# Kernel optimization log

Hardware: AMD Instinct MI355X
Metric: run time of the kernel (lower is better)

## Reference

```python
import jax, jax.numpy as jnp
import numpy as np

N_QUBITS = 12
BATCH = 2048
N_CLASSES = 10


def build_tape(n):
    # 2 layers of: RX on all wires (id 0), RY (id 1), RZ (id 2), then a CRX ring
    # (id 4 forward in layer 0, id 5 reversed in layer 1). 96 gates total for n=12.
    tape = []
    for layer in range(2):
        for i in range(n):
            tape.append(("rx", (i,)))
        for i in range(n):
            tape.append(("ry", (i,)))
        for i in range(n):
            tape.append(("rz", (i,)))
        order = range(n) if layer == 0 else range(n - 1, -1, -1)
        for i in order:
            tape.append(("crx", (i, (i + 1) % n)))
    return tape


def rx_mat(t):
    c = jnp.cos(t / 2).astype(jnp.complex64)
    s = jnp.sin(t / 2).astype(jnp.complex64)
    return jnp.stack([jnp.stack([c, -1j * s]), jnp.stack([-1j * s, c])])


def ry_mat(t):
    c = jnp.cos(t / 2).astype(jnp.complex64)
    s = jnp.sin(t / 2).astype(jnp.complex64)
    return jnp.stack([jnp.stack([c, -s]), jnp.stack([s, c])])


def rz_mat(t):
    em = jnp.exp(-1j * t.astype(jnp.complex64) / 2)
    ep = jnp.exp(1j * t.astype(jnp.complex64) / 2)
    z = jnp.zeros((), jnp.complex64)
    return jnp.stack([jnp.stack([em, z]), jnp.stack([z, ep])])


def apply_1q(psi, U, w):
    # psi: [B] + [2]*n, gate on wire w (axis 1+w)
    psi = jnp.moveaxis(psi, 1 + w, -1)
    psi = psi @ U.T
    return jnp.moveaxis(psi, -1, 1 + w)


def apply_crx(psi, theta, c, t):
    a_c, a_t = 1 + c, 1 + t
    psi = jnp.moveaxis(psi, a_c, 1)  # control -> axis 1
    if a_t < a_c:
        a_t += 1
    psi = jnp.moveaxis(psi, a_t, -1)  # target -> last axis
    U = rx_mat(theta)
    p1 = psi[:, 1] @ U.T  # apply RX only on control=1 branch
    psi = jnp.stack([psi[:, 0], p1], axis=1)
    psi = jnp.moveaxis(psi, -1, a_t)
    return jnp.moveaxis(psi, 1, a_c)


def expvals(psi, n):
    # <X_i>, <Y_i>, <Z_i> for each qubit; returns [B, 3n] ordered X..Y..Z (PL order)
    xs, ys, zs = [], [], []
    for i in range(n):
        p = jnp.moveaxis(psi, 1 + i, -1).reshape(psi.shape[0], -1, 2)
        z = jnp.sum(jnp.abs(p[..., 0]) ** 2 - jnp.abs(p[..., 1]) ** 2, axis=1)
        cross = jnp.sum(jnp.conj(p[..., 0]) * p[..., 1], axis=1)
        xs.append(2.0 * jnp.real(cross))
        ys.append(2.0 * jnp.imag(cross))
        zs.append(jnp.real(z))
    return jnp.stack(xs + ys + zs, axis=1).astype(jnp.float32)


def setup_inputs() -> dict:
    key = jax.random.key(0)
    k0, k1, k2 = jax.random.split(key, 3)
    sv = jax.random.normal(k0, (BATCH, 2 ** N_QUBITS), dtype=jnp.float32)
    sv = sv / jnp.linalg.norm(sv, axis=1, keepdims=True)  # valid quantum states
    n_gates = len(build_tape(N_QUBITS))
    angles = jax.random.normal(k1, (n_gates,), dtype=jnp.float32)
    W = jax.random.normal(k2, (N_CLASSES, 3 * N_QUBITS), dtype=jnp.float32) * 0.1
    b = jnp.zeros((N_CLASSES,), jnp.float32)
    return {"state_vectors": sv, "angles": angles, "W": W, "b": b}


def reference(state_vectors, angles, W, b):
    tape = build_tape(N_QUBITS)
    psi = state_vectors.astype(jnp.complex64).reshape((-1,) + (2,) * N_QUBITS)
    for g, (kind, wires) in enumerate(tape):
        th = angles[g]
        if kind == "rx":
            psi = apply_1q(psi, rx_mat(th), wires[0])
        elif kind == "ry":
            psi = apply_1q(psi, ry_mat(th), wires[0])
        elif kind == "rz":
            psi = apply_1q(psi, rz_mat(th), wires[0])
        else:
            psi = apply_crx(psi, th, wires[0], wires[1])
    feats = expvals(psi, N_QUBITS)  # [B, 3*n_qubits]
    return feats @ W.T + b
```

## Files before the change

### kernel.cpp

```cpp
#include <hip/hip_runtime.h>

#define DIM 4096
using F2 = float2;
using F8 = __attribute__((ext_vector_type(8))) float;
using F2V = __attribute__((ext_vector_type(2))) float;


__device__ __forceinline__ F8 sld8(const float* p) {
    F8 r;
    asm volatile("s_load_dwordx8 %0, %1, 0x0\n\ts_waitcnt lgkmcnt(0)"
                 : "=s"(r) : "s"(p));
    return r;
}
__device__ __forceinline__ void sld16(const float* pa, const float* pb, F8& a, F8& b) {
    asm volatile("s_load_dwordx8 %0, %2, 0x0\n\t"
                 "s_load_dwordx8 %1, %3, 0x0\n\t"
                 "s_waitcnt lgkmcnt(0)"
                 : "=&s"(a), "=&s"(b) : "s"(pa), "s"(pb));
}
__device__ __forceinline__ F2 sld2(const float* p) {
    F2V r;
    asm volatile("s_load_dwordx2 %0, %1, 0x0\n\ts_waitcnt lgkmcnt(0)"
                 : "=s"(r) : "s"(p));
    return F2{r[0], r[1]};
}

__device__ __forceinline__ F2 pk_mul_bl(F2 a, F2 u) {
    F2 d;
    asm("v_pk_mul_f32 %0, %1, %2 op_sel:[0,0] op_sel_hi:[1,0]"
        : "=v"(d) : "v"(a), "s"(u));
    return d;
}
__device__ __forceinline__ void pk_cross(F2& d, F2 a, F2 u) {
    asm("v_pk_fma_f32 %0, %1, %2, %0 op_sel:[1,1,0] op_sel_hi:[0,1,1] neg_lo:[1,0,0]"
        : "+v"(d) : "v"(a), "s"(u));
}
__device__ __forceinline__ void pk_fma_bl(F2& d, F2 a, F2 u) {
    asm("v_pk_fma_f32 %0, %1, %2, %0 op_sel:[0,0,0] op_sel_hi:[1,0,1]"
        : "+v"(d) : "v"(a), "s"(u));
}
__device__ __forceinline__ void pk_swapneg(F2& d, F2 a, F2 cs) {
    asm("v_pk_fma_f32 %0, %1, %2, %0 op_sel:[1,1,0] op_sel_hi:[0,1,1] neg_hi:[1,0,0]"
        : "+v"(d) : "v"(a), "s"(cs));
}
__device__ __forceinline__ void pk_fma(F2& d, F2 a, F2 b) {
    asm("v_pk_fma_f32 %0, %1, %2, %0" : "+v"(d) : "v"(a), "v"(b));
}
__device__ __forceinline__ void pk_imacc(F2& d, F2 a0, F2 a1) {
    asm("v_pk_fma_f32 %0, %1, %2, %0 op_sel:[0,1,0] op_sel_hi:[1,0,1] neg_hi:[1,0,0]"
        : "+v"(d) : "v"(a0), "v"(a1));
}
__device__ __forceinline__ F2 pk_cmul(F2 u, F2 a) {
    F2 d = pk_mul_bl(a, u);
    pk_cross(d, a, u);
    return d;
}
__device__ __forceinline__ void pk_cfma(F2& d, F2 u, F2 a) {
    pk_fma_bl(d, a, u);
    pk_cross(d, a, u);
}

__device__ __forceinline__ void build_u(float tx, float ty, float tz, float* u) {
    float sx = sinf(0.5f*tx), cx = cosf(0.5f*tx);
    float sy = sinf(0.5f*ty), cy = cosf(0.5f*ty);
    float sz = sinf(0.5f*tz), cz = cosf(0.5f*tz);
    float A00r = cy*cx, A00i =  sy*sx;
    float A01r = -sy*cx, A01i = -cy*sx;
    float A10r =  sy*cx, A10i = -cy*sx;
    float A11r =  cy*cx, A11i = -sy*sx;
    u[0] = cz*A00r + sz*A00i;  u[1] = cz*A00i - sz*A00r;
    u[2] = cz*A01r + sz*A01i;  u[3] = cz*A01i - sz*A01r;
    u[4] = cz*A10r - sz*A10i;  u[5] = cz*A10i + sz*A10r;
    u[6] = cz*A11r - sz*A11i;  u[7] = cz*A11i + sz*A11r;
}

__global__ void prep_kernel(const float* __restrict__ ang, float* __restrict__ coef) {
    int t = threadIdx.x;
    if (t < 12) {
        float u[8]; build_u(ang[t], ang[12+t], ang[24+t], u);
#pragma unroll
        for (int j = 0; j < 8; ++j) coef[t*8 + j] = u[j];
    } else if (t < 24) {
        int q = t - 12;
        float u[8]; build_u(ang[48+q], ang[60+q], ang[72+q], u);
#pragma unroll
        for (int j = 0; j < 8; ++j) coef[192 + q*8 + j] = u[j];
    } else if (t < 36) {
        int c = t - 24;
        float th = 0.5f * ang[95 - c];
        coef[296 + c*2]     = cosf(th);
        coef[296 + c*2 + 1] = sinf(th);
    } else if (t < 47) {
        int q = t - 35;
        float u[8]; build_u(ang[q], ang[12+q], ang[24+q], u);
        float c = cosf(0.5f*ang[36+q-1]), s = sinf(0.5f*ang[36+q-1]);
        float m[8];
        m[0] = c*u[0] + s*u[5];  m[1] = c*u[1] - s*u[4];
        m[2] = c*u[2] + s*u[7];  m[3] = c*u[3] - s*u[6];
        m[4] = s*u[1] + c*u[4];  m[5] = -s*u[0] + c*u[5];
        m[6] = s*u[3] + c*u[6];  m[7] = -s*u[2] + c*u[7];
#pragma unroll
        for (int j = 0; j < 8; ++j) coef[96 + q*8 + j] = m[j];
    } else if (t == 47) {
        float u[8]; build_u(ang[48], ang[60], ang[72], u);
        float c = cosf(0.5f*ang[47]), s = sinf(0.5f*ang[47]);
        float m[8];
        m[0] = c*u[0] + s*u[3];  m[1] = c*u[1] - s*u[2];
        m[2] = s*u[1] + c*u[2];  m[3] = -s*u[0] + c*u[3];
        m[4] = c*u[4] + s*u[7];  m[5] = c*u[5] - s*u[6];
        m[6] = s*u[5] + c*u[6];  m[7] = -s*u[4] + c*u[7];
#pragma unroll
        for (int j = 0; j < 8; ++j) coef[288 + j] = m[j];
    }
}

__device__ __forceinline__ int rpA1(int r) {
    int a11=(r>>3)&1, a10=(r>>2)&1, a9=(r>>1)&1;
    return (a11<<8)|(a10<<7)|(a9<<6)|(a11<<3)|(a10<<2)|(a9<<1)|(a9<<0);
}
__device__ __forceinline__ int rpB1(int r) {
    int a5=(r>>1)&1, a7=(r>>2)&1, a6=(r>>3)&1;
    return (a7<<5)|(a6<<4)|(a7<<3)|(a6<<2)|(a5<<0);
}
__device__ __forceinline__ int rpB2(int r) {
    int a8=r&1, a7=(r>>2)&1, a6=(r>>3)&1;
    return (a8<<5)|(a7<<4)|(a6<<3)|(a7<<2)|(a8<<1)|(a6<<0);
}
__device__ __forceinline__ int rpC2(int r) {
    int a2=r&1, a4=(r>>2)&1, a3=(r>>3)&1;
    return (a3<<3)|(a2<<2)|(a4<<1);
}
__device__ __forceinline__ int rpC3(int r) {
    int a5=(r>>1)&1, a4=(r>>2)&1, a3=(r>>3)&1;
    return (a5<<4)|(a3<<3)|(a4<<2)|(a5<<0);
}
__device__ __forceinline__ int rpD3(int r) {
    int a1=(r>>1)&1, a0=(r>>2)&1, a11=(r>>3)&1;
    return (a11<<8)|(a11<<3)|(a1<<1)|((a0^a11)<<0);
}
__device__ __forceinline__ int rpC5(int r) {
    int a2=r&1, a4=(r>>2)&1, a3=(r>>3)&1;
    return (a4<<4)|(a3<<3)|(a2<<2)|(a4<<0);
}
__device__ __forceinline__ int rpB5(int r) {
    int a8=r&1, a7=(r>>2)&1, a6=(r>>3)&1;
    return (a7<<10)|(a6<<9)|(a8<<5)|(a8<<3);
}

#define LBITS \
    const int l0=l&1, l1=(l>>1)&1, l2=(l>>2)&1, l3=(l>>3)&1, l4=(l>>4)&1, \
              l5=(l>>5)&1, w0=w&1, w1=(w>>1)&1; \
    (void)l0;(void)l1;(void)l2;(void)l3;(void)l4;(void)l5;(void)w0;(void)w1;

__device__ __forceinline__ int tpA1f(int l, int w) { LBITS
    return (w1<<10)|(w0<<9)|(l5<<5)|(l4<<4)|((l1^l5)<<3)|((l0^l4)<<2)|(l2<<1)|(l3<<0); }
__device__ __forceinline__ int tpB1f(int l, int w) { LBITS
    return (w1<<10)|(w0<<9)|(l5<<8)|(l4<<7)|(l3<<6)|((l1^l5)<<3)|((l0^l4)<<2)|((l2^l3)<<1)|(l3<<0); }
__device__ __forceinline__ int tpC2f(int l, int w) { LBITS
    return (w1<<10)|(w0<<9)|(l5<<8)|(l4<<7)|(l3<<6)|(l2<<5)|(l1<<4)|((l5^l0)<<3)|((l4^l1)<<2)|((l3^l2)<<1)|((l0^l3)<<0); }
__device__ __forceinline__ int tpC3f(int l, int w) { LBITS
    return (l1<<10)|(l0<<9)|(l5<<8)|(l4<<7)|(l3<<6)|(l2<<5)|((l5^l4)<<3)|(l3<<2)|((w1^l2)<<1)|((w0^l5)<<0); }
__device__ __forceinline__ int tpD3f(int l, int w) { LBITS
    return (w1<<10)|(w0<<9)|(l5<<7)|(l4<<6)|(l3<<5)|(l2<<4)|((l0^l5)<<3)|((l1^l4)<<2)|(l3<<1)|(l2<<0); }
__device__ __forceinline__ int tpC4f(int l, int w) { LBITS
    return (w1<<10)|(w0<<9)|(l5<<8)|(l4<<7)|(l3<<6)|(l2<<5)|((l5^l4)<<3)|(l3<<2)|((l1^l2)<<1)|((l0^l5)<<0); }
__device__ __forceinline__ int tpC5f(int l, int w) { LBITS
    return (w1<<10)|(w0<<9)|(l5<<8)|(l4<<7)|(l3<<6)|(l2<<5)|((l5^l2)<<3)|(l4<<2)|((l1^l3)<<1)|(l0<<0); }
__device__ __forceinline__ int tpB5f(int l, int w) { LBITS
    return (l5<<8)|(l4<<7)|(l3<<6)|(l2<<4)|((l1^l5)<<3)|((l0^l4)<<2)|((w1^l3)<<1)|((w0^l2)<<0); }

template<int M, int S1, int H1>
__device__ __forceinline__ void g1q(F2* amp, F2 u00, F2 u01, F2 u10, F2 u11) {
#pragma unroll
    for (int r0 = 0; r0 < 16; ++r0) {
        if (r0 & M) continue;
        if (S1 != 0 && (r0 & S1) != H1) continue;
        const int r1 = r0 + M;
        F2 a0 = amp[r0], a1 = amp[r1];
        F2 n0 = pk_cmul(u00, a0); pk_cfma(n0, u01, a1);
        F2 n1 = pk_cmul(u10, a0); pk_cfma(n1, u11, a1);
        amp[r0] = n0; amp[r1] = n1;
    }
}
template<int M, int S1, int H1>
__device__ __forceinline__ void g1qF(F2* amp, F8 u) {
    g1q<M, S1, H1>(amp, F2{u[0],u[1]}, F2{u[2],u[3]}, F2{u[4],u[5]}, F2{u[6],u[7]});
}

template<int MSEL, int M, int S1, int H1>
__device__ __forceinline__ void fg1q(F2* amp, F2 a00, F2 a01, F2 a10, F2 a11,
                                     F2 b00, F2 b01, F2 b10, F2 b11) {
#pragma unroll
    for (int r0 = 0; r0 < 16; ++r0) {
        if (r0 & M) continue;
        if (S1 != 0 && (r0 & S1) != H1) continue;
        const int r1 = r0 + M;
        const bool sel = (r0 & MSEL) != 0;
        F2 u00 = sel ? b00 : a00, u01 = sel ? b01 : a01;
        F2 u10 = sel ? b10 : a10, u11 = sel ? b11 : a11;
        F2 a0 = amp[r0], a1 = amp[r1];
        F2 n0 = pk_cmul(u00, a0); pk_cfma(n0, u01, a1);
        F2 n1 = pk_cmul(u10, a0); pk_cfma(n1, u11, a1);
        amp[r0] = n0; amp[r1] = n1;
    }
}
template<int MSEL, int M, int S1, int H1>
__device__ __forceinline__ void fg1qF(F2* amp, F8 a, F8 b) {
    fg1q<MSEL, M, S1, H1>(amp,
        F2{a[0],a[1]}, F2{a[2],a[3]}, F2{a[4],a[5]}, F2{a[6],a[7]},
        F2{b[0],b[1]}, F2{b[2],b[3]}, F2{b[4],b[5]}, F2{b[6],b[7]});
}

template<int MC, int MT>
__device__ __forceinline__ void crx(F2* amp, F2 cs) {
#pragma unroll
    for (int r0 = 0; r0 < 16; ++r0) {
        if (!(r0 & MC) || (r0 & MT)) continue;
        const int r1 = r0 + MT;
        F2 a0 = amp[r0], a1 = amp[r1];
        F2 n0 = pk_mul_bl(a0, cs); pk_swapneg(n0, a1, cs);
        F2 n1 = pk_mul_bl(a1, cs); pk_swapneg(n1, a0, cs);
        amp[r0] = n0; amp[r1] = n1;
    }
}

template<int M>
__device__ __forceinline__ void expv(const F2* amp, int q, int lane,
                                     float& fx, float& fy, float& fz) {
    F2 zp = {0.f, 0.f}, zm = {0.f, 0.f}, xp = {0.f, 0.f}, ip = {0.f, 0.f};
#pragma unroll
    for (int r0 = 0; r0 < 16; ++r0) {
        if (r0 & M) continue;
        const int r1 = r0 + M;
        F2 a0 = amp[r0], a1 = amp[r1];
        pk_fma(zp, a0, a0);
        pk_fma(zm, a1, a1);
        pk_fma(xp, a0, a1);
        pk_imacc(ip, a0, a1);
    }
    float zz = (zp.x + zp.y) - (zm.x + zm.y);
    float xr = 2.f * (xp.x + xp.y);
    float xi = 2.f * (ip.x + ip.y);
#pragma unroll
    for (int off = 32; off; off >>= 1) {
        xr += __shfl_xor(xr, off);
        xi += __shfl_xor(xi, off);
        zz += __shfl_xor(zz, off);
    }
    if (lane == q) { fx = xr; fy = xi; fz = zz; }
}

template<int M, int SB>
__device__ __forceinline__ int r0_of(int j, int hb) {
    int r = hb ? SB : 0, b = 1;
#pragma unroll
    for (int p = 0; p < 4; ++p) {
        const int mm = 1 << p;
        if (mm == M || mm == SB) continue;
        if (j & b) r |= mm;
        b <<= 1;
    }
    return r;
}

#define ST_T(TP, RP, SB, HB) \
  { _Pragma("unroll") for (int r = 0; r < 16; ++r) { \
      if ((r & (SB)) != (HB)) continue; \
      psi[(TP) ^ RP(r)] = amp[r]; } }
#define LD_T(TP, RP, M, SB, HB) \
  { _Pragma("unroll") for (int k = 0; k < 8; ++k) { \
      const int j = k >> 1; \
      const int r0 = r0_of<M, SB>(j, (HB) != 0); \
      const int r = (k & 1) ? (r0 + (M)) : r0; \
      amp[r] = psi[(TP) ^ RP(r)]; } }

#define U0P(q, M)    g1qF<M, 0, 0>(amp, sld8(cf + (q)*8))
#define FU0(q, MS, M) do { F8 ua_, ub_; sld16(cf + (q)*8, cf + 96 + (q)*8, ua_, ub_); \
                           fg1qF<MS, M, 0, 0>(amp, ua_, ub_); } while(0)
#define U1P(q, M)    g1qF<M, 0, 0>(amp, sld8(cf + 192 + (q)*8))
#define FU1_0()      do { F8 ua_, ub_; sld16(cf + 192, cf + 288, ua_, ub_); \
                          fg1qF<4, 8, 0, 0>(amp, ua_, ub_); } while(0)
#define CR1(c, MC, MT) crx<MC, MT>(amp, sld2(cf + 296 + (c)*2))
#define EXPV(q, M)   expv<M>(amp, q, l, fx, fy, fz)

__global__ __launch_bounds__(256, 1)
void qsim_kernel(const float* __restrict__ sv,
                 const float* __restrict__ cf,
                 const float* __restrict__ W,
                 const float* __restrict__ bvec,
                 float* __restrict__ out)
{
    __shared__ F2 psi[2048];
    const int t = threadIdx.x;
    const int b = blockIdx.x;
    const int l = t & 63, w = t >> 6;

    F2 amp[16];
    const float* svb = sv + (size_t)b * DIM;
#pragma unroll
    for (int k = 0; k < 16; ++k) {
        const int r = (k & 1) ? ((k >> 1) + 8) : (k >> 1);
        amp[r] = make_float2(svb[(r << 8) | (l << 2) | w], 0.f);
    }

    float fx = 0.f, fy = 0.f, fz = 0.f;

    U0P(0, 8);
    FU0(1, 8, 4); FU0(2, 4, 2); FU0(3, 2, 1);

    {
        F8 ua, ub; sld16(cf + 4*8, cf + 96 + 4*8, ua, ub);
        const int tpA = tpA1f(l, w), tpB = tpB1f(l, w);
        ST_T(tpA, rpA1, 1, 0);
        LD_T(tpB, rpB1, 4, 1, 0);
        ST_T(tpA, rpA1, 1, 1);
        fg1qF<1, 4, 1, 0>(amp, ua, ub);
        LD_T(tpB, rpB1, 4, 1, 1);
        fg1qF<1, 4, 1, 1>(amp, ua, ub);
    }
    FU0(5, 4, 8); FU0(6, 8, 2);

    {
        F8 ua, ub; sld16(cf + 7*8, cf + 96 + 7*8, ua, ub);
        const int tpB = tpB1f(l, w), tpC = tpC2f(l, w);
        ST_T(tpB, rpB2, 2, 0);
        LD_T(tpC, rpC2, 4, 2, 0);
        ST_T(tpB, rpB2, 2, 2);
        fg1qF<2, 4, 2, 0>(amp, ua, ub);
        LD_T(tpC, rpC2, 4, 2, 2);
        fg1qF<2, 4, 2, 2>(amp, ua, ub);
    }
    FU0(8, 4, 8); FU0(9, 8, 1);

    {
        F8 ua, ub; sld16(cf + 10*8, cf + 96 + 10*8, ua, ub);
        __syncthreads();
        const int tpC = tpC3f(l, w), tpD = tpD3f(l, w);
        ST_T(tpC, rpC3, 1, 0);
        __syncthreads();
        LD_T(tpD, rpD3, 2, 1, 0);
        __syncthreads();
        ST_T(tpC, rpC3, 1, 1);
        fg1qF<1, 2, 1, 0>(amp, ua, ub);
        __syncthreads();
        LD_T(tpD, rpD3, 2, 1, 1);
        fg1qF<1, 2, 1, 1>(amp, ua, ub);
    }
    FU0(11, 2, 4);
    FU1_0();
    U1P(9, 1); U1P(10, 2); U1P(11, 4);
    CR1(11, 4, 8); CR1(10, 2, 4); CR1(9, 1, 2);
    EXPV(10, 2); EXPV(11, 4);

    {
        F8 u7 = sld8(cf + 192 + 7*8);
        const int tpD = tpD3f(l, w), tpC = tpC4f(l, w);
        ST_T(tpD, rpD3, 1, 0);
        LD_T(tpC, rpC3, 4, 1, 0);
        ST_T(tpD, rpD3, 1, 1);
        g1qF<4, 1, 0>(amp, u7);
        LD_T(tpC, rpC3, 4, 1, 1);
        g1qF<4, 1, 1>(amp, u7);
    }
    U1P(6, 2); U1P(8, 8);
    CR1(8, 8, 1); CR1(7, 4, 8); CR1(6, 2, 4);
    EXPV(9, 1); EXPV(8, 8); EXPV(7, 4);

    {
        F8 u3 = sld8(cf + 192 + 3*8);
        const int tpC = tpC5f(l, w), tpB = tpB5f(l, w);
        ST_T(tpC, rpC5, 2, 0);
        __syncthreads();
        LD_T(tpB, rpB5, 1, 2, 0);
        __syncthreads();
        ST_T(tpC, rpC5, 2, 2);
        g1qF<1, 2, 0>(amp, u3);
        __syncthreads();
        LD_T(tpB, rpB5, 1, 2, 2);
        g1qF<1, 2, 2>(amp, u3);
        __syncthreads();
    }
    U1P(4, 4); U1P(5, 8);
    CR1(5, 8, 2); CR1(4, 4, 8); CR1(3, 1, 4);
    EXPV(6, 2); EXPV(5, 8); EXPV(4, 4);

    {
        F8 u1 = sld8(cf + 192 + 1*8);
        const int tpB = tpB1f(l, w), tpA = tpA1f(l, w);
        ST_T(tpB, rpB1, 1, 0);
        LD_T(tpA, rpA1, 4, 1, 0);
        ST_T(tpB, rpB1, 1, 1);
        g1qF<4, 1, 0>(amp, u1);
        LD_T(tpA, rpA1, 4, 1, 1);
        g1qF<4, 1, 1>(amp, u1);
    }
    U1P(2, 2);
    CR1(2, 2, 1); CR1(1, 4, 2); CR1(0, 8, 4);
    EXPV(3, 1); EXPV(2, 2); EXPV(1, 4); EXPV(0, 8);

    __syncthreads();
    float* fbuf = (float*)psi;
    if (l < 12) {
        fbuf[w * 36 + l]      = fx;
        fbuf[w * 36 + 12 + l] = fy;
        fbuf[w * 36 + 24 + l] = fz;
    }
    __syncthreads();
    if (t < 10) {
        float a = bvec[t];
#pragma unroll
        for (int f = 0; f < 36; ++f)
            a += W[t * 36 + f] * (fbuf[f] + fbuf[36 + f] + fbuf[72 + f] + fbuf[108 + f]);
        out[(size_t)b * 10 + t] = a;
    }
}

extern "C" void kernel_launch(void* const* d_in, const int* in_sizes, int n_in,
                              void* d_out, int out_size, void* d_ws, size_t ws_size,
                              hipStream_t stream) {
    const float* sv     = (const float*)d_in[0];
    const float* angles = (const float*)d_in[1];
    const float* W      = (const float*)d_in[2];
    const float* bvec   = (const float*)d_in[3];
    float* out  = (float*)d_out;
    float* coef = (float*)d_ws;
    int batch = in_sizes[0] / DIM;
    prep_kernel<<<1, 64, 0, stream>>>(angles, coef);
    qsim_kernel<<<batch, 256, 0, stream>>>(sv, coef, W, bvec, out);
}
```

Measured before the change: 133.9 us.

## Process two batch samples per block to amortize coefficient loads and syncs

Each block now simulates two state vectors at once, using two register amplitude arrays and two shared-memory buffers. Gate coefficients loaded through scalar loads and the block barriers are shared across both samples, and the interleaved independent work should expose more instruction-level parallelism. In exchange the launch uses half as many blocks (1024 on 256 CUs), register pressure doubles, and shared memory doubles. It also assumes an even batch size.

```diff
diff --git a/kernel.cpp b/kernel.cpp
--- a/kernel.cpp
+++ b/kernel.cpp
@@ -263,25 +263,31 @@
     return r;
 }
 
-#define ST_T(TP, RP, SB, HB) \
+#define ST_T(AMP, PS, TP, RP, SB, HB) \
   { _Pragma("unroll") for (int r = 0; r < 16; ++r) { \
       if ((r & (SB)) != (HB)) continue; \
-      psi[(TP) ^ RP(r)] = amp[r]; } }
-#define LD_T(TP, RP, M, SB, HB) \
+      (PS)[(TP) ^ RP(r)] = AMP[r]; } }
+#define LD_T(AMP, PS, TP, RP, M, SB, HB) \
   { _Pragma("unroll") for (int k = 0; k < 8; ++k) { \
       const int j = k >> 1; \
       const int r0 = r0_of<M, SB>(j, (HB) != 0); \
       const int r = (k & 1) ? (r0 + (M)) : r0; \
-      amp[r] = psi[(TP) ^ RP(r)]; } }
-
-#define U0P(q, M)    g1qF<M, 0, 0>(amp, sld8(cf + (q)*8))
+      AMP[r] = (PS)[(TP) ^ RP(r)]; } }
+
+#define U0P(q, M)    do { F8 u_ = sld8(cf + (q)*8); \
+                          g1qF<M, 0, 0>(amp0, u_); g1qF<M, 0, 0>(amp1, u_); } while(0)
 #define FU0(q, MS, M) do { F8 ua_, ub_; sld16(cf + (q)*8, cf + 96 + (q)*8, ua_, ub_); \
-                           fg1qF<MS, M, 0, 0>(amp, ua_, ub_); } while(0)
-#define U1P(q, M)    g1qF<M, 0, 0>(amp, sld8(cf + 192 + (q)*8))
+                           fg1qF<MS, M, 0, 0>(amp0, ua_, ub_); \
+                           fg1qF<MS, M, 0, 0>(amp1, ua_, ub_); } while(0)
+#define U1P(q, M)    do { F8 u_ = sld8(cf + 192 + (q)*8); \
+                          g1qF<M, 0, 0>(amp0, u_); g1qF<M, 0, 0>(amp1, u_); } while(0)
 #define FU1_0()      do { F8 ua_, ub_; sld16(cf + 192, cf + 288, ua_, ub_); \
-                          fg1qF<4, 8, 0, 0>(amp, ua_, ub_); } while(0)
-#define CR1(c, MC, MT) crx<MC, MT>(amp, sld2(cf + 296 + (c)*2))
-#define EXPV(q, M)   expv<M>(amp, q, l, fx, fy, fz)
+                          fg1qF<4, 8, 0, 0>(amp0, ua_, ub_); \
+                          fg1qF<4, 8, 0, 0>(amp1, ua_, ub_); } while(0)
+#define CR1(c, MC, MT) do { F2 cs_ = sld2(cf + 296 + (c)*2); \
+                            crx<MC, MT>(amp0, cs_); crx<MC, MT>(amp1, cs_); } while(0)
+#define EXPV(q, M)   do { expv<M>(amp0, q, l, fx0, fy0, fz0); \
+                          expv<M>(amp1, q, l, fx1, fy1, fz1); } while(0)
 
 __global__ __launch_bounds__(256, 1)
 void qsim_kernel(const float* __restrict__ sv,
@@ -290,20 +296,25 @@
                  const float* __restrict__ bvec,
                  float* __restrict__ out)
 {
-    __shared__ F2 psi[2048];
+    __shared__ F2 psi[4096];
+    F2* const psi1 = psi + 2048;
     const int t = threadIdx.x;
     const int b = blockIdx.x;
     const int l = t & 63, w = t >> 6;
 
-    F2 amp[16];
-    const float* svb = sv + (size_t)b * DIM;
+    F2 amp0[16], amp1[16];
+    const float* svb0 = sv + (size_t)(2 * b) * DIM;
+    const float* svb1 = svb0 + DIM;
 #pragma unroll
     for (int k = 0; k < 16; ++k) {
         const int r = (k & 1) ? ((k >> 1) + 8) : (k >> 1);
-        amp[r] = make_float2(svb[(r << 8) | (l << 2) | w], 0.f);
-    }
-
-    float fx = 0.f, fy = 0.f, fz = 0.f;
+        const int idx = (r << 8) | (l << 2) | w;
+        amp0[r] = make_float2(svb0[idx], 0.f);
+        amp1[r] = make_float2(svb1[idx], 0.f);
+    }
+
+    float fx0 = 0.f, fy0 = 0.f, fz0 = 0.f;
+    float fx1 = 0.f, fy1 = 0.f, fz1 = 0.f;
 
     U0P(0, 8);
     FU0(1, 8, 4); FU0(2, 4, 2); FU0(3, 2, 1);
@@ -311,24 +322,36 @@
     {
         F8 ua, ub; sld16(cf + 4*8, cf + 96 + 4*8, ua, ub);
         const int tpA = tpA1f(l, w), tpB = tpB1f(l, w);
-        ST_T(tpA, rpA1, 1, 0);
-        LD_T(tpB, rpB1, 4, 1, 0);
-        ST_T(tpA, rpA1, 1, 1);
-        fg1qF<1, 4, 1, 0>(amp, ua, ub);
-        LD_T(tpB, rpB1, 4, 1, 1);
-        fg1qF<1, 4, 1, 1>(amp, ua, ub);
+        ST_T(amp0, psi,  tpA, rpA1, 1, 0);
+        ST_T(amp1, psi1, tpA, rpA1, 1, 0);
+        LD_T(amp0, psi,  tpB, rpB1, 4, 1, 0);
+        LD_T(amp1, psi1, tpB, rpB1, 4, 1, 0);
+        ST_T(amp0, psi,  tpA, rpA1, 1, 1);
+        ST_T(amp1, psi1, tpA, rpA1, 1, 1);
+        fg1qF<1, 4, 1, 0>(amp0, ua, ub);
+        fg1qF<1, 4, 1, 0>(amp1, ua, ub);
+        LD_T(amp0, psi,  tpB, rpB1, 4, 1, 1);
+        LD_T(amp1, psi1, tpB, rpB1, 4, 1, 1);
+        fg1qF<1, 4, 1, 1>(amp0, ua, ub);
+        fg1qF<1, 4, 1, 1>(amp1, ua, ub);
     }
     FU0(5, 4, 8); FU0(6, 8, 2);
 
     {
         F8 ua, ub; sld16(cf + 7*8, cf + 96 + 7*8, ua, ub);
         const int tpB = tpB1f(l, w), tpC = tpC2f(l, w);
-        ST_T(tpB, rpB2, 2, 0);
-        LD_T(tpC, rpC2, 4, 2, 0);
-        ST_T(tpB, rpB2, 2, 2);
-        fg1qF<2, 4, 2, 0>(amp, ua, ub);
-        LD_T(tpC, rpC2, 4, 2, 2);
-        fg1qF<2, 4, 2, 2>(amp, ua, ub);
+        ST_T(amp0, psi,  tpB, rpB2, 2, 0);
+        ST_T(amp1, psi1, tpB, rpB2, 2, 0);
+        LD_T(amp0, psi,  tpC, rpC2, 4, 2, 0);
+        LD_T(amp1, psi1, tpC, rpC2, 4, 2, 0);
+        ST_T(amp0, psi,  tpB, rpB2, 2, 2);
+        ST_T(amp1, psi1, tpB, rpB2, 2, 2);
+        fg1qF<2, 4, 2, 0>(amp0, ua, ub);
+        fg1qF<2, 4, 2, 0>(amp1, ua, ub);
+        LD_T(amp0, psi,  tpC, rpC2, 4, 2, 2);
+        LD_T(amp1, psi1, tpC, rpC2, 4, 2, 2);
+        fg1qF<2, 4, 2, 2>(amp0, ua, ub);
+        fg1qF<2, 4, 2, 2>(amp1, ua, ub);
     }
     FU0(8, 4, 8); FU0(9, 8, 1);
 
@@ -336,15 +359,21 @@
         F8 ua, ub; sld16(cf + 10*8, cf + 96 + 10*8, ua, ub);
         __syncthreads();
         const int tpC = tpC3f(l, w), tpD = tpD3f(l, w);
-        ST_T(tpC, rpC3, 1, 0);
-        __syncthreads();
-        LD_T(tpD, rpD3, 2, 1, 0);
-        __syncthreads();
-        ST_T(tpC, rpC3, 1, 1);
-        fg1qF<1, 2, 1, 0>(amp, ua, ub);
-        __syncthreads();
-        LD_T(tpD, rpD3, 2, 1, 1);
-        fg1qF<1, 2, 1, 1>(amp, ua, ub);
+        ST_T(amp0, psi,  tpC, rpC3, 1, 0);
+        ST_T(amp1, psi1, tpC, rpC3, 1, 0);
+        __syncthreads();
+        LD_T(amp0, psi,  tpD, rpD3, 2, 1, 0);
+        LD_T(amp1, psi1, tpD, rpD3, 2, 1, 0);
+        __syncthreads();
+        ST_T(amp0, psi,  tpC, rpC3, 1, 1);
+        ST_T(amp1, psi1, tpC, rpC3, 1, 1);
+        fg1qF<1, 2, 1, 0>(amp0, ua, ub);
+        fg1qF<1, 2, 1, 0>(amp1, ua, ub);
+        __syncthreads();
+        LD_T(amp0, psi,  tpD, rpD3, 2, 1, 1);
+        LD_T(amp1, psi1, tpD, rpD3, 2, 1, 1);
+        fg1qF<1, 2, 1, 1>(amp0, ua, ub);
+        fg1qF<1, 2, 1, 1>(amp1, ua, ub);
     }
     FU0(11, 2, 4);
     FU1_0();
@@ -355,12 +384,18 @@
     {
         F8 u7 = sld8(cf + 192 + 7*8);
         const int tpD = tpD3f(l, w), tpC = tpC4f(l, w);
-        ST_T(tpD, rpD3, 1, 0);
-        LD_T(tpC, rpC3, 4, 1, 0);
-        ST_T(tpD, rpD3, 1, 1);
-        g1qF<4, 1, 0>(amp, u7);
-        LD_T(tpC, rpC3, 4, 1, 1);
-        g1qF<4, 1, 1>(amp, u7);
+        ST_T(amp0, psi,  tpD, rpD3, 1, 0);
+        ST_T(amp1, psi1, tpD, rpD3, 1, 0);
+        LD_T(amp0, psi,  tpC, rpC3, 4, 1, 0);
+        LD_T(amp1, psi1, tpC, rpC3, 4, 1, 0);
+        ST_T(amp0, psi,  tpD, rpD3, 1, 1);
+        ST_T(amp1, psi1, tpD, rpD3, 1, 1);
+        g1qF<4, 1, 0>(amp0, u7);
+        g1qF<4, 1, 0>(amp1, u7);
+        LD_T(amp0, psi,  tpC, rpC3, 4, 1, 1);
+        LD_T(amp1, psi1, tpC, rpC3, 4, 1, 1);
+        g1qF<4, 1, 1>(amp0, u7);
+        g1qF<4, 1, 1>(amp1, u7);
     }
     U1P(6, 2); U1P(8, 8);
     CR1(8, 8, 1); CR1(7, 4, 8); CR1(6, 2, 4);
@@ -369,15 +404,21 @@
     {
         F8 u3 = sld8(cf + 192 + 3*8);
         const int tpC = tpC5f(l, w), tpB = tpB5f(l, w);
-        ST_T(tpC, rpC5, 2, 0);
-        __syncthreads();
-        LD_T(tpB, rpB5, 1, 2, 0);
-        __syncthreads();
-        ST_T(tpC, rpC5, 2, 2);
-        g1qF<1, 2, 0>(amp, u3);
-        __syncthreads();
-        LD_T(tpB, rpB5, 1, 2, 2);
-        g1qF<1, 2, 2>(amp, u3);
+        ST_T(amp0, psi,  tpC, rpC5, 2, 0);
+        ST_T(amp1, psi1, tpC, rpC5, 2, 0);
+        __syncthreads();
+        LD_T(amp0, psi,  tpB, rpB5, 1, 2, 0);
+        LD_T(amp1, psi1, tpB, rpB5, 1, 2, 0);
+        __syncthreads();
+        ST_T(amp0, psi,  tpC, rpC5, 2, 2);
+        ST_T(amp1, psi1, tpC, rpC5, 2, 2);
+        g1qF<1, 2, 0>(amp0, u3);
+        g1qF<1, 2, 0>(amp1, u3);
+        __syncthreads();
+        LD_T(amp0, psi,  tpB, rpB5, 1, 2, 2);
+        LD_T(amp1, psi1, tpB, rpB5, 1, 2, 2);
+        g1qF<1, 2, 2>(amp0, u3);
+        g1qF<1, 2, 2>(amp1, u3);
         __syncthreads();
     }
     U1P(4, 4); U1P(5, 8);
@@ -387,12 +428,18 @@
     {
         F8 u1 = sld8(cf + 192 + 1*8);
         const int tpB = tpB1f(l, w), tpA = tpA1f(l, w);
-        ST_T(tpB, rpB1, 1, 0);
-        LD_T(tpA, rpA1, 4, 1, 0);
-        ST_T(tpB, rpB1, 1, 1);
-        g1qF<4, 1, 0>(amp, u1);
-        LD_T(tpA, rpA1, 4, 1, 1);
-        g1qF<4, 1, 1>(amp, u1);
+        ST_T(amp0, psi,  tpB, rpB1, 1, 0);
+        ST_T(amp1, psi1, tpB, rpB1, 1, 0);
+        LD_T(amp0, psi,  tpA, rpA1, 4, 1, 0);
+        LD_T(amp1, psi1, tpA, rpA1, 4, 1, 0);
+        ST_T(amp0, psi,  tpB, rpB1, 1, 1);
+        ST_T(amp1, psi1, tpB, rpB1, 1, 1);
+        g1qF<4, 1, 0>(amp0, u1);
+        g1qF<4, 1, 0>(amp1, u1);
+        LD_T(amp0, psi,  tpA, rpA1, 4, 1, 1);
+        LD_T(amp1, psi1, tpA, rpA1, 4, 1, 1);
+        g1qF<4, 1, 1>(amp0, u1);
+        g1qF<4, 1, 1>(amp1, u1);
     }
     U1P(2, 2);
     CR1(2, 2, 1); CR1(1, 4, 2); CR1(0, 8, 4);
@@ -401,17 +448,20 @@
     __syncthreads();
     float* fbuf = (float*)psi;
     if (l < 12) {
-        fbuf[w * 36 + l]      = fx;
-        fbuf[w * 36 + 12 + l] = fy;
-        fbuf[w * 36 + 24 + l] = fz;
+        float* f0 = fbuf + w * 36;
+        f0[l] = fx0;  f0[12 + l] = fy0;  f0[24 + l] = fz0;
+        float* f1 = fbuf + 144 + w * 36;
+        f1[l] = fx1;  f1[12 + l] = fy1;  f1[24 + l] = fz1;
     }
     __syncthreads();
-    if (t < 10) {
-        float a = bvec[t];
+    if (t < 20) {
+        const int s = t / 10, row = t % 10;
+        const float* fb = fbuf + s * 144;
+        float a = bvec[row];
 #pragma unroll
         for (int f = 0; f < 36; ++f)
-            a += W[t * 36 + f] * (fbuf[f] + fbuf[36 + f] + fbuf[72 + f] + fbuf[108 + f]);
-        out[(size_t)b * 10 + t] = a;
+            a += W[row * 36 + f] * (fb[f] + fb[36 + f] + fb[72 + f] + fb[108 + f]);
+        out[(size_t)(2 * b + s) * 10 + row] = a;
     }
 }
 
@@ -426,5 +476,5 @@
     float* coef = (float*)d_ws;
     int batch = in_sizes[0] / DIM;
     prep_kernel<<<1, 64, 0, stream>>>(angles, coef);
-    qsim_kernel<<<batch, 256, 0, stream>>>(sv, coef, W, bvec, out);
-}
+    qsim_kernel<<<batch / 2, 256, 0, stream>>>(sv, coef, W, bvec, out);
+}
```

Result: slower. 147.8 us (+10.3%).
